# Kernel optimization log

Hardware: AMD Instinct MI355X
Metric: run time of the kernel (lower is better)

Reference implementation:

```python
import jax, jax.numpy as jnp
import numpy as np

N_NODES = 50000
N_EDGES = 800000
F = 64      # node feature channels (irreps_out = 64x0e)
L = 4       # edge spherical-harmonic dim (lmax=1)
R = 8       # radial basis size
H = 64      # radial MLP hidden
AVG_NUM_NEIGHBOURS = 16.0


def setup_inputs() -> dict:
    key = jax.random.key(0)
    ks = jax.random.split(key, 10)
    node_features = jax.random.normal(ks[0], (N_NODES, F), jnp.float32)
    edge_features = jax.random.normal(ks[1], (N_EDGES, L), jnp.float32)
    radial_embedding = jax.random.uniform(ks[2], (N_EDGES, R), jnp.float32)
    senders = jax.random.randint(ks[3], (N_EDGES,), 0, N_NODES)
    receivers = jax.random.randint(ks[4], (N_EDGES,), 0, N_NODES)
    edge_mask = jnp.ones((N_EDGES,), jnp.bool_)
    W_up = jax.random.normal(ks[5], (F, F), jnp.float32) / np.sqrt(F)
    W1 = jax.random.normal(ks[6], (R, H), jnp.float32) / np.sqrt(R)
    W2 = jax.random.normal(ks[7], (H, H), jnp.float32) / np.sqrt(H)
    W3 = jax.random.normal(ks[8], (H, F * L), jnp.float32) / np.sqrt(H)
    W_down = jax.random.normal(ks[9], (F, F), jnp.float32) / np.sqrt(F)
    return dict(node_features=node_features, edge_features=edge_features,
                radial_embedding=radial_embedding, senders=senders,
                receivers=receivers, edge_mask=edge_mask,
                W_up=W_up, W1=W1, W2=W2, W3=W3, W_down=W_down)


def reference(node_features, edge_features, radial_embedding, senders,
              receivers, edge_mask, W_up, W1, W2, W3, W_down):
    n_nodes = node_features.shape[0]
    # linear_up
    x = node_features @ W_up  # [N, F]
    # radial MLP -> per-edge, per-(channel, l) tensor-product path weights
    h = jax.nn.swish(radial_embedding @ W1)
    h = jax.nn.swish(h @ W2)
    w = (h @ W3).reshape(-1, F, L)  # [E, F, L]
    # gather sender features, weighted tensor product with edge attrs,
    # contracted over the edge-attribute (spherical-harmonic) axis
    x_s = x[senders]  # [E, F]
    msg = jnp.einsum('ef,el,efl->ef', x_s, edge_features, w)  # [E, F]
    msg = jnp.where(edge_mask[:, None], msg, jnp.zeros((), msg.dtype))
    # scatter-add to receivers and normalize
    agg = jax.ops.segment_sum(msg, receivers, num_segments=n_nodes)
    agg = agg / AVG_NUM_NEIGHBOURS
    # linear_down
    return agg @ W_down
```

## Files before the change

kernel.cpp:

```cpp
#include <hip/hip_runtime.h>
#include <hip/hip_bf16.h>

typedef _Float16 half8 __attribute__((ext_vector_type(8)));
typedef _Float16 half4v __attribute__((ext_vector_type(4)));
typedef float f32x4 __attribute__((ext_vector_type(4)));

#define NN 50000
#define NE 800000

__device__ __forceinline__ float swishf(float v) {
  return v * __builtin_amdgcn_rcpf(1.f + __expf(-v));
}

__global__ void pack_kernel(const float* __restrict__ W3, const float* __restrict__ W2,
                            _Float16* __restrict__ w3p, _Float16* __restrict__ w2p) {
  const int b = blockIdx.x, tid = threadIdx.x;
  if (b < 8) {
    int t = b * 256 + tid;
    int lane = t & 63, nt = (t >> 6) & 3, ks = t >> 8;
    int f = 16 * nt + (lane & 15);
    int jb = 32 * ks + 8 * (lane >> 4);
#pragma unroll
    for (int u = 0; u < 8; ++u) {
      int j = jb + u;
      w3p[t * 8 + u] = (_Float16)W3[(j >> 2) * 256 + 4 * f + (j & 3)];
    }
  } else {
    int t = (b - 8) * 256 + tid;
    if (t < 512) {
      int lane = t & 63, nt = (t >> 6) & 3, kk = t >> 8;
      int c = 16 * nt + (lane & 15);
      int kb = 32 * kk + 8 * (lane >> 4);
#pragma unroll
      for (int u = 0; u < 8; ++u)
        w2p[t * 8 + u] = (_Float16)W2[(kb + u) * 64 + c];
    }
  }
}

__global__ __launch_bounds__(256)
void linear_up_kernel(const float* __restrict__ X, const float* __restrict__ W,
                      _Float16* __restrict__ Y) {
  int gid = blockIdx.x * 256 + (int)threadIdx.x;
  int row = gid >> 6;
  int lane = threadIdx.x & 63;
  const float* xr = X + (long)row * 64;
  float acc = 0.f;
#pragma unroll
  for (int k = 0; k < 64; ++k) acc = fmaf(xr[k], W[k * 64 + lane], acc);
  Y[(long)row * 64 + lane] = (_Float16)acc;
}

__global__ void hist_kernel(const int* __restrict__ rcv, int* __restrict__ deg) {
  int e = blockIdx.x * 256 + threadIdx.x;
  if (e < NE) atomicAdd(&deg[rcv[e]], 1);
}

__global__ __launch_bounds__(256)
void scan1_kernel(const int* __restrict__ deg, int* __restrict__ bsum) {
  __shared__ int s[256];
  int gid = blockIdx.x * 256 + threadIdx.x;
  s[threadIdx.x] = (gid < NN) ? deg[gid] : 0;
  __syncthreads();
  for (int d = 128; d > 0; d >>= 1) {
    if (threadIdx.x < d) s[threadIdx.x] += s[threadIdx.x + d];
    __syncthreads();
  }
  if (threadIdx.x == 0) bsum[blockIdx.x] = s[0];
}

__global__ __launch_bounds__(256)
void scan2_kernel(const int* __restrict__ bsum, int* __restrict__ boff) {
  __shared__ int s[256];
  int t = threadIdx.x;
  int v = (t < 196) ? bsum[t] : 0;
  s[t] = v;
  __syncthreads();
  for (int d = 1; d < 256; d <<= 1) {
    int x = (t >= d) ? s[t - d] : 0;
    __syncthreads();
    s[t] += x;
    __syncthreads();
  }
  boff[t] = s[t] - v;
}

__global__ __launch_bounds__(256)
void scan3_kernel(const int* __restrict__ deg, const int* __restrict__ boff,
                  int* __restrict__ pos, int* __restrict__ cur) {
  __shared__ int s[256];
  int t = threadIdx.x, gid = blockIdx.x * 256 + t;
  int v = (gid < NN) ? deg[gid] : 0;
  s[t] = v;
  __syncthreads();
  for (int d = 1; d < 256; d <<= 1) {
    int x = (t >= d) ? s[t - d] : 0;
    __syncthreads();
    s[t] += x;
    __syncthreads();
  }
  int ex = s[t] - v + boff[blockIdx.x];
  if (gid < NN) {
    pos[gid] = ex;
    cur[gid] = ex;
    if (gid == NN - 1) pos[NN] = ex + v;
  }
}

__global__ __launch_bounds__(256, 4)
void fused_tp_kernel(const float* __restrict__ rad, const float* __restrict__ ef,
                     const _Float16* __restrict__ xup, const int* __restrict__ snd,
                     const int* __restrict__ rcv, const int* __restrict__ msk,
                     const float* __restrict__ W1,
                     const _Float16* __restrict__ w2p, const _Float16* __restrict__ w3p,
                     int* __restrict__ cur, _Float16* __restrict__ msg) {
  __shared__ float    s_ef[128][4];
  __shared__ _Float16 s_xs[128][72];
  __shared__ _Float16 s_hp[128][72];
  __shared__ int      s_slot[128];

  const int t = threadIdx.x;
  const long e0 = (long)blockIdx.x * 128;
  const int w = t >> 6, lane = t & 63, m = lane & 15, g = lane >> 4;
  const int ew0 = 32 * w;

  {
    const float2 e2 = *reinterpret_cast<const float2*>(ef + (e0 + ew0) * 4 + lane * 2);
    const int rr = ew0 + (lane >> 1), rc = 2 * (lane & 1);
    s_ef[rr][rc] = e2.x;
    s_ef[rr][rc + 1] = e2.y;
    if (lane < 32) s_slot[ew0 + lane] = atomicAdd(&cur[rcv[e0 + ew0 + lane]], 1);
    const int e = ew0 + (lane >> 1), q2 = lane & 1;
    const int sn = snd[e0 + e];
    const int mk = msk[e0 + e];
    uint4 v0 = {0,0,0,0}, v1 = {0,0,0,0}, v2 = {0,0,0,0}, v3 = {0,0,0,0};
    if (mk) {
      const uint4* src = reinterpret_cast<const uint4*>(xup + (long)sn * 64 + q2 * 32);
      v0 = src[0]; v1 = src[1]; v2 = src[2]; v3 = src[3];
    }
    uint4* dst = reinterpret_cast<uint4*>(&s_xs[e][q2 * 32]);
    dst[0] = v0; dst[1] = v1; dst[2] = v2; dst[3] = v3;
  }

  const int em0 = ew0 + m;
  const int em1 = ew0 + 16 + m;

  float rv0[8], rv1[8];
  {
    const float4 a = *reinterpret_cast<const float4*>(rad + (e0 + em0) * 8);
    const float4 b = *reinterpret_cast<const float4*>(rad + (e0 + em0) * 8 + 4);
    const float4 c = *reinterpret_cast<const float4*>(rad + (e0 + em1) * 8);
    const float4 d = *reinterpret_cast<const float4*>(rad + (e0 + em1) * 8 + 4);
    rv0[0]=a.x; rv0[1]=a.y; rv0[2]=a.z; rv0[3]=a.w;
    rv0[4]=b.x; rv0[5]=b.y; rv0[6]=b.z; rv0[7]=b.w;
    rv1[0]=c.x; rv1[1]=c.y; rv1[2]=c.z; rv1[3]=c.w;
    rv1[4]=d.x; rv1[5]=d.y; rv1[6]=d.z; rv1[7]=d.w;
  }

  half8 af0[2], af1[2];
#pragma unroll
  for (int kk = 0; kk < 2; ++kk) {
    float a0[8], a1[8];
#pragma unroll
    for (int u = 0; u < 8; ++u) { a0[u] = 0.f; a1[u] = 0.f; }
#pragma unroll
    for (int k = 0; k < 8; ++k) {
      const float4 wa = *reinterpret_cast<const float4*>(W1 + k * 64 + 32 * kk + 8 * g);
      const float4 wb = *reinterpret_cast<const float4*>(W1 + k * 64 + 32 * kk + 8 * g + 4);
      a0[0] = fmaf(rv0[k], wa.x, a0[0]);  a1[0] = fmaf(rv1[k], wa.x, a1[0]);
      a0[1] = fmaf(rv0[k], wa.y, a0[1]);  a1[1] = fmaf(rv1[k], wa.y, a1[1]);
      a0[2] = fmaf(rv0[k], wa.z, a0[2]);  a1[2] = fmaf(rv1[k], wa.z, a1[2]);
      a0[3] = fmaf(rv0[k], wa.w, a0[3]);  a1[3] = fmaf(rv1[k], wa.w, a1[3]);
      a0[4] = fmaf(rv0[k], wb.x, a0[4]);  a1[4] = fmaf(rv1[k], wb.x, a1[4]);
      a0[5] = fmaf(rv0[k], wb.y, a0[5]);  a1[5] = fmaf(rv1[k], wb.y, a1[5]);
      a0[6] = fmaf(rv0[k], wb.z, a0[6]);  a1[6] = fmaf(rv1[k], wb.z, a1[6]);
      a0[7] = fmaf(rv0[k], wb.w, a0[7]);  a1[7] = fmaf(rv1[k], wb.w, a1[7]);
    }
#pragma unroll
    for (int u = 0; u < 8; ++u) {
      af0[kk][u] = (_Float16)swishf(a0[u]);
      af1[kk][u] = (_Float16)swishf(a1[u]);
    }
  }

  {
    half8 bw[8];
#pragma unroll
    for (int i = 0; i < 8; ++i)
      bw[i] = *reinterpret_cast<const half8*>(w2p + ((size_t)i * 64 + lane) * 8);

    f32x4 A0[4], A1[4];
#pragma unroll
    for (int nt = 0; nt < 4; ++nt) { A0[nt] = (f32x4){0.f,0.f,0.f,0.f}; A1[nt] = (f32x4){0.f,0.f,0.f,0.f}; }
#pragma unroll
    for (int kk = 0; kk < 2; ++kk) {
#pragma unroll
      for (int nt = 0; nt < 4; ++nt) {
        A0[nt] = __builtin_amdgcn_mfma_f32_16x16x32_f16(af0[kk], bw[kk * 4 + nt], A0[nt], 0, 0, 0);
        A1[nt] = __builtin_amdgcn_mfma_f32_16x16x32_f16(af1[kk], bw[kk * 4 + nt], A1[nt], 0, 0, 0);
      }
    }
    const int col = lane & 15, rg = lane >> 4;
    const int pbase = 16 * ((col >> 1) & 3) + 2 * (col >> 3) + (col & 1);
#pragma unroll
    for (int nt = 0; nt < 4; ++nt) {
      const int pos = pbase + 4 * nt;
#pragma unroll
      for (int i = 0; i < 4; ++i) {
        const int r0 = ew0 + rg * 4 + i;
        s_hp[r0][pos]      = (_Float16)swishf(A0[nt][i]);
        s_hp[r0 + 16][pos] = (_Float16)swishf(A1[nt][i]);
      }
    }
  }

  {
    const _Float16* hr0 = &s_hp[em0][g * 16];
    const _Float16* hr1 = &s_hp[em1][g * 16];
    half8 hlo0 = *reinterpret_cast<const half8*>(hr0);
    half8 hhi0 = *reinterpret_cast<const half8*>(hr0 + 8);
    half8 hlo1 = *reinterpret_cast<const half8*>(hr1);
    half8 hhi1 = *reinterpret_cast<const half8*>(hr1 + 8);

    _Float16 ef0[4], ef1[4];
#pragma unroll
    for (int l = 0; l < 4; ++l) {
      ef0[l] = (_Float16)s_ef[em0][l];
      ef1[l] = (_Float16)s_ef[em1][l];
    }

    f32x4 c0[4], c1[4];
#pragma unroll
    for (int nt = 0; nt < 4; ++nt) { c0[nt] = (f32x4){0.f,0.f,0.f,0.f}; c1[nt] = (f32x4){0.f,0.f,0.f,0.f}; }

#pragma unroll
    for (int ks = 0; ks < 8; ++ks) {
      half8 bfr[4];
#pragma unroll
      for (int nt = 0; nt < 4; ++nt)
        bfr[nt] = *reinterpret_cast<const half8*>(w3p + ((size_t)(ks * 4 + nt) * 64 + lane) * 8);

      const _Float16 p0  = (ks < 4) ? hlo0[2 * ks]     : hhi0[2 * (ks - 4)];
      const _Float16 p1  = (ks < 4) ? hlo0[2 * ks + 1] : hhi0[2 * (ks - 4) + 1];
      const _Float16 q0  = (ks < 4) ? hlo1[2 * ks]     : hhi1[2 * (ks - 4)];
      const _Float16 q1  = (ks < 4) ? hlo1[2 * ks + 1] : hhi1[2 * (ks - 4) + 1];
      half8 a0, a1;
#pragma unroll
      for (int l = 0; l < 4; ++l) {
        a0[l]     = p0 * ef0[l];
        a0[4 + l] = p1 * ef0[l];
        a1[l]     = q0 * ef1[l];
        a1[4 + l] = q1 * ef1[l];
      }
#pragma unroll
      for (int nt = 0; nt < 4; ++nt) {
        c0[nt] = __builtin_amdgcn_mfma_f32_16x16x32_f16(a0, bfr[nt], c0[nt], 0, 0, 0);
        c1[nt] = __builtin_amdgcn_mfma_f32_16x16x32_f16(a1, bfr[nt], c1[nt], 0, 0, 0);
      }
    }

    const int col = lane & 15, rg = lane >> 4;
#pragma unroll
    for (int nt = 0; nt < 4; ++nt) {
      const int f = nt * 16 + col;
#pragma unroll
      for (int i = 0; i < 4; ++i) {
        const int r0 = ew0 + rg * 4 + i;
        s_hp[r0][f]      = (_Float16)(c0[nt][i] * (float)s_xs[r0][f]);
        s_hp[r0 + 16][f] = (_Float16)(c1[nt][i] * (float)s_xs[r0 + 16][f]);
      }
    }
  }

  {
    const int e = ew0 + (lane >> 1), q2 = lane & 1;
    const uint4* src = reinterpret_cast<const uint4*>(&s_hp[e][q2 * 32]);
    uint4 v0 = src[0], v1 = src[1], v2 = src[2], v3 = src[3];
    uint4* dst = reinterpret_cast<uint4*>(msg + (long)s_slot[e] * 64 + q2 * 32);
    dst[0] = v0; dst[1] = v1; dst[2] = v2; dst[3] = v3;
  }
}

__global__ __launch_bounds__(256, 8)
void gather_down_kernel(const _Float16* __restrict__ msg, const int* __restrict__ pos,
                        const float* __restrict__ W_dn, float* __restrict__ out) {
  __shared__ int   s_pos[17];
  __shared__ float s_agg[16][65];

  const int t = threadIdx.x;
  const int node0 = blockIdx.x * 16;

  if (t < 17) s_pos[t] = pos[node0 + t];
  __syncthreads();

  const int tg = t >> 4, tl = t & 15;
  float a0 = 0.f, a1 = 0.f, a2 = 0.f, a3 = 0.f;
  for (int a = s_pos[tg]; a < s_pos[tg + 1]; ++a) {
    half4v v = *reinterpret_cast<const half4v*>(msg + (long)a * 64 + tl * 4);
    a0 += (float)v[0]; a1 += (float)v[1]; a2 += (float)v[2]; a3 += (float)v[3];
  }
  s_agg[tg][tl * 4 + 0] = a0;
  s_agg[tg][tl * 4 + 1] = a1;
  s_agg[tg][tl * 4 + 2] = a2;
  s_agg[tg][tl * 4 + 3] = a3;
  __syncthreads();

  {
    const int r = t >> 4, c0 = (t & 15) * 4;
    float b0 = 0.f, b1 = 0.f, b2 = 0.f, b3 = 0.f;
    for (int k = 0; k < 64; ++k) {
      const float x = s_agg[r][k];
      const float4 wv = *reinterpret_cast<const float4*>(W_dn + k * 64 + c0);
      b0 = fmaf(x, wv.x, b0);
      b1 = fmaf(x, wv.y, b1);
      b2 = fmaf(x, wv.z, b2);
      b3 = fmaf(x, wv.w, b3);
    }
    float4 o = { b0 * 0.0625f, b1 * 0.0625f, b2 * 0.0625f, b3 * 0.0625f };
    *reinterpret_cast<float4*>(out + (long)(node0 + r) * 64 + c0) = o;
  }
}

extern "C" void kernel_launch(void* const* d_in, const int* in_sizes, int n_in,
                              void* d_out, int out_size, void* d_ws, size_t ws_size,
                              hipStream_t stream) {
  const float* nf   = (const float*)d_in[0];
  const float* ef   = (const float*)d_in[1];
  const float* rad  = (const float*)d_in[2];
  const int*   snd  = (const int*)d_in[3];
  const int*   rcv  = (const int*)d_in[4];
  const int*   msk  = (const int*)d_in[5];
  const float* W_up = (const float*)d_in[6];
  const float* W1   = (const float*)d_in[7];
  const float* W2   = (const float*)d_in[8];
  const float* W3   = (const float*)d_in[9];
  const float* W_dn = (const float*)d_in[10];
  float* out = (float*)d_out;

  _Float16* msg  = (_Float16*)d_ws;
  _Float16* xbuf = msg + (size_t)NE * 64;
  _Float16* w3p  = xbuf + (size_t)NN * 64;
  _Float16* w2p  = w3p + 2048 * 8;
  int*      deg  = (int*)(w2p + 512 * 8);
  int*      pos  = deg + NN;
  int*      cur  = pos + NN + 1;
  int*      bsum = cur + NN;
  int*      boff = bsum + 256;

  hipMemsetAsync(deg, 0, (size_t)NN * sizeof(int), stream);

  hist_kernel<<<NE / 256, 256, 0, stream>>>(rcv, deg);
  scan1_kernel<<<196, 256, 0, stream>>>(deg, bsum);
  scan2_kernel<<<1, 256, 0, stream>>>(bsum, boff);
  scan3_kernel<<<196, 256, 0, stream>>>(deg, boff, pos, cur);

  pack_kernel<<<10, 256, 0, stream>>>(W3, W2, w3p, w2p);
  linear_up_kernel<<<(NN * 64) / 256, 256, 0, stream>>>(nf, W_up, xbuf);

  fused_tp_kernel<<<NE / 128, 256, 0, stream>>>(rad, ef, xbuf, snd, rcv, msk,
                                                W1, w2p, w3p, cur, msg);

  gather_down_kernel<<<NN / 16, 256, 0, stream>>>(msg, pos, W_dn, out);
}
```

Before: 245.5 us.

## Write messages in edge order with index permutation and merge prep kernels

Fuses linear_up, degree histogram and weight packing into a single prep kernel to reduce launches. The fused TP kernel now writes messages contiguously by edge id and records a receiver-sorted edge index permutation instead of scattering message rows to sorted slots. The gather kernel reads messages indirectly through that permutation. This trades scattered writes for scattered reads plus an extra index load per edge.

New measurement: 248.4 us. No clear change (+1.2%).

```diff
diff --git a/kernel.cpp b/kernel.cpp
--- a/kernel.cpp
+++ b/kernel.cpp
@@ -12,48 +12,48 @@
   return v * __builtin_amdgcn_rcpf(1.f + __expf(-v));
 }
 
-__global__ void pack_kernel(const float* __restrict__ W3, const float* __restrict__ W2,
-                            _Float16* __restrict__ w3p, _Float16* __restrict__ w2p) {
+__global__ __launch_bounds__(256)
+void prep_kernel(const float* __restrict__ nf, const float* __restrict__ W_up,
+                 _Float16* __restrict__ xbuf, const int* __restrict__ rcv,
+                 int* __restrict__ deg, const float* __restrict__ W3,
+                 const float* __restrict__ W2, _Float16* __restrict__ w3p,
+                 _Float16* __restrict__ w2p) {
   const int b = blockIdx.x, tid = threadIdx.x;
-  if (b < 8) {
-    int t = b * 256 + tid;
-    int lane = t & 63, nt = (t >> 6) & 3, ks = t >> 8;
-    int f = 16 * nt + (lane & 15);
-    int jb = 32 * ks + 8 * (lane >> 4);
-#pragma unroll
-    for (int u = 0; u < 8; ++u) {
-      int j = jb + u;
-      w3p[t * 8 + u] = (_Float16)W3[(j >> 2) * 256 + 4 * f + (j & 3)];
-    }
+  if (b < 12500) {
+    const int gid = b * 256 + tid;
+    const int row = gid >> 6, lane = tid & 63;
+    const float* xr = nf + (long)row * 64;
+    float acc = 0.f;
+#pragma unroll
+    for (int k = 0; k < 64; ++k) acc = fmaf(xr[k], W_up[k * 64 + lane], acc);
+    xbuf[(long)row * 64 + lane] = (_Float16)acc;
+  } else if (b < 15625) {
+    const int e = (b - 12500) * 256 + tid;
+    atomicAdd(&deg[rcv[e]], 1);
   } else {
-    int t = (b - 8) * 256 + tid;
-    if (t < 512) {
-      int lane = t & 63, nt = (t >> 6) & 3, kk = t >> 8;
-      int c = 16 * nt + (lane & 15);
-      int kb = 32 * kk + 8 * (lane >> 4);
-#pragma unroll
-      for (int u = 0; u < 8; ++u)
-        w2p[t * 8 + u] = (_Float16)W2[(kb + u) * 64 + c];
-    }
-  }
-}
-
-__global__ __launch_bounds__(256)
-void linear_up_kernel(const float* __restrict__ X, const float* __restrict__ W,
-                      _Float16* __restrict__ Y) {
-  int gid = blockIdx.x * 256 + (int)threadIdx.x;
-  int row = gid >> 6;
-  int lane = threadIdx.x & 63;
-  const float* xr = X + (long)row * 64;
-  float acc = 0.f;
-#pragma unroll
-  for (int k = 0; k < 64; ++k) acc = fmaf(xr[k], W[k * 64 + lane], acc);
-  Y[(long)row * 64 + lane] = (_Float16)acc;
-}
-
-__global__ void hist_kernel(const int* __restrict__ rcv, int* __restrict__ deg) {
-  int e = blockIdx.x * 256 + threadIdx.x;
-  if (e < NE) atomicAdd(&deg[rcv[e]], 1);
+    const int bb = b - 15625;
+    if (bb < 8) {
+      int t = bb * 256 + tid;
+      int lane = t & 63, nt = (t >> 6) & 3, ks = t >> 8;
+      int f = 16 * nt + (lane & 15);
+      int jb = 32 * ks + 8 * (lane >> 4);
+#pragma unroll
+      for (int u = 0; u < 8; ++u) {
+        int j = jb + u;
+        w3p[t * 8 + u] = (_Float16)W3[(j >> 2) * 256 + 4 * f + (j & 3)];
+      }
+    } else {
+      int t = (bb - 8) * 256 + tid;
+      if (t < 512) {
+        int lane = t & 63, nt = (t >> 6) & 3, kk = t >> 8;
+        int c = 16 * nt + (lane & 15);
+        int kb = 32 * kk + 8 * (lane >> 4);
+#pragma unroll
+        for (int u = 0; u < 8; ++u)
+          w2p[t * 8 + u] = (_Float16)W2[(kb + u) * 64 + c];
+      }
+    }
+  }
 }
 
 __global__ __launch_bounds__(256)
@@ -113,11 +113,11 @@
                      const int* __restrict__ rcv, const int* __restrict__ msk,
                      const float* __restrict__ W1,
                      const _Float16* __restrict__ w2p, const _Float16* __restrict__ w3p,
-                     int* __restrict__ cur, _Float16* __restrict__ msg) {
+                     int* __restrict__ cur, int* __restrict__ eidx,
+                     _Float16* __restrict__ msg) {
   __shared__ float    s_ef[128][4];
   __shared__ _Float16 s_xs[128][72];
   __shared__ _Float16 s_hp[128][72];
-  __shared__ int      s_slot[128];
 
   const int t = threadIdx.x;
   const long e0 = (long)blockIdx.x * 128;
@@ -129,7 +129,11 @@
     const int rr = ew0 + (lane >> 1), rc = 2 * (lane & 1);
     s_ef[rr][rc] = e2.x;
     s_ef[rr][rc + 1] = e2.y;
-    if (lane < 32) s_slot[ew0 + lane] = atomicAdd(&cur[rcv[e0 + ew0 + lane]], 1);
+    if (lane < 32) {
+      const int ea = (int)e0 + ew0 + lane;
+      const int slot = atomicAdd(&cur[rcv[ea]], 1);
+      eidx[slot] = ea;
+    }
     const int e = ew0 + (lane >> 1), q2 = lane & 1;
     const int sn = snd[e0 + e];
     const int mk = msk[e0 + e];
@@ -276,14 +280,15 @@
     const int e = ew0 + (lane >> 1), q2 = lane & 1;
     const uint4* src = reinterpret_cast<const uint4*>(&s_hp[e][q2 * 32]);
     uint4 v0 = src[0], v1 = src[1], v2 = src[2], v3 = src[3];
-    uint4* dst = reinterpret_cast<uint4*>(msg + (long)s_slot[e] * 64 + q2 * 32);
+    uint4* dst = reinterpret_cast<uint4*>(msg + (e0 + e) * 64 + q2 * 32);
     dst[0] = v0; dst[1] = v1; dst[2] = v2; dst[3] = v3;
   }
 }
 
 __global__ __launch_bounds__(256, 8)
-void gather_down_kernel(const _Float16* __restrict__ msg, const int* __restrict__ pos,
-                        const float* __restrict__ W_dn, float* __restrict__ out) {
+void gather_down_kernel(const _Float16* __restrict__ msg, const int* __restrict__ eidx,
+                        const int* __restrict__ pos, const float* __restrict__ W_dn,
+                        float* __restrict__ out) {
   __shared__ int   s_pos[17];
   __shared__ float s_agg[16][65];
 
@@ -296,7 +301,8 @@
   const int tg = t >> 4, tl = t & 15;
   float a0 = 0.f, a1 = 0.f, a2 = 0.f, a3 = 0.f;
   for (int a = s_pos[tg]; a < s_pos[tg + 1]; ++a) {
-    half4v v = *reinterpret_cast<const half4v*>(msg + (long)a * 64 + tl * 4);
+    const int eid = eidx[a];
+    half4v v = *reinterpret_cast<const half4v*>(msg + (long)eid * 64 + tl * 4);
     a0 += (float)v[0]; a1 += (float)v[1]; a2 += (float)v[2]; a3 += (float)v[3];
   }
   s_agg[tg][tl * 4 + 0] = a0;
@@ -341,7 +347,8 @@
   _Float16* xbuf = msg + (size_t)NE * 64;
   _Float16* w3p  = xbuf + (size_t)NN * 64;
   _Float16* w2p  = w3p + 2048 * 8;
-  int*      deg  = (int*)(w2p + 512 * 8);
+  int*      eidx = (int*)(w2p + 512 * 8);
+  int*      deg  = eidx + NE;
   int*      pos  = deg + NN;
   int*      cur  = pos + NN + 1;
   int*      bsum = cur + NN;
@@ -349,16 +356,14 @@
 
   hipMemsetAsync(deg, 0, (size_t)NN * sizeof(int), stream);
 
-  hist_kernel<<<NE / 256, 256, 0, stream>>>(rcv, deg);
+  prep_kernel<<<15635, 256, 0, stream>>>(nf, W_up, xbuf, rcv, deg, W3, W2, w3p, w2p);
+
   scan1_kernel<<<196, 256, 0, stream>>>(deg, bsum);
   scan2_kernel<<<1, 256, 0, stream>>>(bsum, boff);
   scan3_kernel<<<196, 256, 0, stream>>>(deg, boff, pos, cur);
 
-  pack_kernel<<<10, 256, 0, stream>>>(W3, W2, w3p, w2p);
-  linear_up_kernel<<<(NN * 64) / 256, 256, 0, stream>>>(nf, W_up, xbuf);
-
   fused_tp_kernel<<<NE / 128, 256, 0, stream>>>(rad, ef, xbuf, snd, rcv, msk,
-                                                W1, w2p, w3p, cur, msg);
-
-  gather_down_kernel<<<NN / 16, 256, 0, stream>>>(msg, pos, W_dn, out);
-}
+                                                W1, w2p, w3p, cur, eidx, msg);
+
+  gather_down_kernel<<<NN / 16, 256, 0, stream>>>(msg, eidx, pos, W_dn, out);
+}
```
